# Performance work log

Hardware: AMD Instinct MI355X
Metric: run time of the kernel (lower is better)

## Reference

```python
import jax, jax.numpy as jnp
import numpy as np
from jax import lax

H = W = 224
FH = FW = 7          # backbone feature map spatial size
THRESH = 0.7
NUM_CLASSES = 14


def _conv(x, w, stride, pad):
    return lax.conv_general_dilated(
        x, w, (stride, stride), [(pad, pad), (pad, pad)],
        dimension_numbers=('NCHW', 'OIHW', 'NCHW'))


def backbone(x, w0, w1, w2, w3, fw, fb):
    # stand-in resnet50 trunk: 224 -> 56 -> 28 -> 14 -> 7, channels 3->64->512->1024->2048
    h = jax.nn.relu(_conv(x, w0, 4, 3))      # [B,64,56,56]
    h = jax.nn.relu(_conv(h, w1, 2, 1))      # [B,512,28,28]
    h = jax.nn.relu(_conv(h, w2, 2, 1))      # [B,1024,14,14]
    feat = jax.nn.relu(_conv(h, w3, 2, 1))   # [B,2048,7,7]
    pool = feat.max(axis=(2, 3))             # MaxPool2d(k=7,s=1) on 7x7 == global max -> [B,2048]
    out = jax.nn.sigmoid(pool @ fw.T + fb)   # fc + Sigmoid -> [B,14]
    return out, feat, pool


def attention_gen_patchs(img, fm):
    B, C, Hh, Ww = img.shape
    # per-sample channel-max abs heatmap, min-max normalized
    hm = jnp.max(jnp.abs(fm), axis=1)                              # [B,7,7]
    mn = hm.min(axis=(1, 2), keepdims=True)
    mx = hm.max(axis=(1, 2), keepdims=True)
    hm = (hm - mn) / (mx - mn)
    hm = jax.image.resize(hm, (B, Hh, Ww), method='bilinear')      # Resize((h,w))
    mask = (hm > THRESH).astype(jnp.int32)                         # [B,H,W]

    # largest 8-connected component: iterative max-label propagation
    ids = jnp.arange(1, Hh * Ww + 1, dtype=jnp.int32).reshape(1, Hh, Ww) * mask
    def body(_, lab):
        p = lax.reduce_window(lab, jnp.int32(0), lax.max, (1, 3, 3), (1, 1, 1), 'SAME')
        return p * mask
    labels = lax.fori_loop(0, Hh + Ww, body, ids)                  # [B,H,W] int32

    def counts_one(lab):
        c = jnp.zeros((Hh * Ww + 1,), jnp.int32).at[lab.reshape(-1)].add(1)
        return c.at[0].set(-1)                                     # ignore background
    counts = jax.vmap(counts_one)(labels)                          # [B,H*W+1]
    max_label = jnp.argmax(counts, axis=1)                         # [B]
    lcc = labels == max_label[:, None, None]                       # [B,H,W] bool

    # bbox of largest component (xmin/xmax over rows, ymin/ymax over cols)
    ri = jnp.arange(Hh); ci = jnp.arange(Ww)
    rows = lcc.any(axis=2); cols = lcc.any(axis=1)
    xmin = jnp.min(jnp.where(rows, ri[None, :], Hh), axis=1)
    xmax = jnp.max(jnp.where(rows, ri[None, :], -1), axis=1)       # inclusive; torch slice excludes it
    ymin = jnp.min(jnp.where(cols, ci[None, :], Ww), axis=1)
    ymax = jnp.max(jnp.where(cols, ci[None, :], -1), axis=1)
    ch = jnp.maximum(xmax - xmin, 1).astype(jnp.float32)           # crop height (exclusive slice)
    cw = jnp.maximum(ymax - ymin, 1).astype(jnp.float32)

    # bilinear resize of crop [xmin:xmax, ymin:ymax] back to (H,W), align_corners=False
    fy0 = xmin.astype(jnp.float32); fx0 = ymin.astype(jnp.float32)
    oy = (jnp.arange(Hh, dtype=jnp.float32) + 0.5)[None, :] * (ch[:, None] / Hh) + fy0[:, None] - 0.5
    ox = (jnp.arange(Ww, dtype=jnp.float32) + 0.5)[None, :] * (cw[:, None] / Ww) + fx0[:, None] - 0.5
    oy = jnp.clip(oy, fy0[:, None], jnp.maximum(fy0 + ch - 1.0, fy0)[:, None])
    ox = jnp.clip(ox, fx0[:, None], jnp.maximum(fx0 + cw - 1.0, fx0)[:, None])

    def sample_one(im, yy, xx):  # im [C,H,W]
        gy = jnp.broadcast_to(yy[:, None], (Hh, Ww))
        gx = jnp.broadcast_to(xx[None, :], (Hh, Ww))
        f = lambda chan: jax.scipy.ndimage.map_coordinates(chan, [gy, gx], order=1, mode='nearest')
        return jax.vmap(f)(im)
    return jax.vmap(sample_one)(img, oy, ox)                       # [B,C,H,W]


def bce(p, t):
    p = jnp.clip(p, 1e-7, 1.0 - 1e-7)
    return -jnp.mean(t * jnp.log(p) + (1.0 - t) * jnp.log1p(-p))


def setup_inputs() -> dict:
    key = jax.random.key(0)
    ks = jax.random.split(key, 20)
    B = 4
    def conv_w(k, o, i, s):
        return jax.random.normal(k, (o, i, s, s), jnp.float32) * np.sqrt(2.0 / (i * s * s)).astype(np.float32)
    def lin(k, o, i):
        return jax.random.normal(k, (o, i), jnp.float32) * np.sqrt(1.0 / i).astype(np.float32)
    inp = {
        'img': jax.random.uniform(ks[0], (B, 3, H, W), jnp.float32),
        'target': jax.random.uniform(ks[1], (B, NUM_CLASSES), jnp.float32),
        'gw0': conv_w(ks[2], 64, 3, 7), 'gw1': conv_w(ks[3], 512, 64, 3),
        'gw2': conv_w(ks[4], 1024, 512, 3), 'gw3': conv_w(ks[5], 2048, 1024, 3),
        'gfw': lin(ks[6], NUM_CLASSES, 2048), 'gfb': jnp.zeros((NUM_CLASSES,), jnp.float32),
        'lw0': conv_w(ks[7], 64, 3, 7), 'lw1': conv_w(ks[8], 512, 64, 3),
        'lw2': conv_w(ks[9], 1024, 512, 3), 'lw3': conv_w(ks[10], 2048, 1024, 3),
        'lfw': lin(ks[11], NUM_CLASSES, 2048), 'lfb': jnp.zeros((NUM_CLASSES,), jnp.float32),
        'fw': lin(ks[12], NUM_CLASSES, 2048 * 2), 'fb': jnp.zeros((NUM_CLASSES,), jnp.float32),
    }
    return inp


def reference(img, target, gw0, gw1, gw2, gw3, gfw, gfb,
              lw0, lw1, lw2, lw3, lfw, lfb, fw, fb):
    out_g, fm_g, pool_g = backbone(img, gw0, gw1, gw2, gw3, gfw, gfb)
    # patch generation is non-differentiable in the original (CPU/PIL round trip)
    patch = attention_gen_patchs(lax.stop_gradient(img), lax.stop_gradient(fm_g))
    out_l, _, pool_l = backbone(patch, lw0, lw1, lw2, lw3, lfw, lfb)
    out_f = jax.nn.sigmoid(jnp.concatenate([pool_g, pool_l], axis=1) @ fw.T + fb)
    gl = bce(out_g, target); ll = bce(out_l, target); fl = bce(out_f, target)
    loss = 0.8 * gl + 0.1 * ll + 0.1 * fl
    return loss, out_g, out_l, out_f, patch
```

## Files before the change

### kernel.cpp

```cpp
#include <hip/hip_runtime.h>
#include <math.h>

typedef __attribute__((ext_vector_type(8))) short short8m;
typedef __attribute__((ext_vector_type(4))) float f32x4;

__device__ inline unsigned short bf16_trunc(float f) {
  return (unsigned short)(__float_as_uint(f) >> 16);
}
__device__ inline unsigned short bf16_rte(float f) {
  unsigned u = __float_as_uint(f);
  u += 0x7fffu + ((u >> 16) & 1u);
  return (unsigned short)(u >> 16);
}
__device__ inline float bf16_tof(unsigned short h) {
  return __uint_as_float(((unsigned)h) << 16);
}
__device__ inline short8m* ldsPtr(unsigned short* base, int row, int byteInRow) {
  int off = (row * 128 + byteInRow) ^ ((row & 7) << 4);
  return (short8m*)((char*)base + off);
}
__device__ inline void gload16_lds(const void* g, void* d) {
  __builtin_amdgcn_global_load_lds((const __attribute__((address_space(1))) unsigned int*)g,
                                   (__attribute__((address_space(3))) unsigned int*)d, 16, 0, 0);
}

__global__ __launch_bounds__(256) void k_conv7(const float* __restrict__ x,
                                               const float* __restrict__ w,
                                               float* __restrict__ y) {
  __shared__ float ws[147];
  const int boc = blockIdx.y;
  const int oc = boc & 63;
  const int b = boc >> 6;
  for (int i = threadIdx.x; i < 147; i += 256) ws[i] = w[oc * 147 + i];
  __syncthreads();
  int px = blockIdx.x * 256 + threadIdx.x;
  if (px >= 56 * 56) return;
  int oy = px / 56, ox = px % 56;
  int iy0 = oy * 4 - 3, ix0 = ox * 4 - 3;
  float acc = 0.f;
  for (int c = 0; c < 3; ++c) {
    const float* xp = x + ((size_t)(b * 3 + c)) * 224 * 224;
    #pragma unroll
    for (int ky = 0; ky < 7; ++ky) {
      int iy = iy0 + ky;
      if ((unsigned)iy < 224u) {
        #pragma unroll
        for (int kx = 0; kx < 7; ++kx) {
          int ix = ix0 + kx;
          if ((unsigned)ix < 224u)
            acc += xp[iy * 224 + ix] * ws[c * 49 + ky * 7 + kx];
        }
      }
    }
  }
  y[((size_t)boc * 56 + oy) * 56 + ox] = fmaxf(acc, 0.f);
}

__global__ __launch_bounds__(256) void k_padw(const float* __restrict__ w,
                                              float* __restrict__ wp,
                                              int kreal, int ktot, int noc) {
  int i = blockIdx.x * 256 + threadIdx.x;
  if (i >= noc * ktot) return;
  int oc = i / ktot, k = i % ktot;
  wp[i] = (k < kreal) ? w[oc * kreal + k] : 0.f;
}

template <int CIN, int HIN, int WIN, int HOUT, int WOUT, int KH, int KW, int STR, int PAD, int KTOT>
__global__ __launch_bounds__(256) void k_im2col(const float* __restrict__ x,
                                                unsigned short* __restrict__ XgH,
                                                unsigned short* __restrict__ XgM) {
  constexpr int NPX = 4 * HOUT * WOUT;
  constexpr int K8 = KTOT / 8;
  constexpr int KK = KH * KW;
  int u = blockIdx.x * 256 + threadIdx.x;
  int pxin = u & 63;
  int k8 = (u >> 6) % K8;
  int pxblk = (u >> 6) / K8;
  int px = pxblk * 64 + pxin;
  if (px > NPX - 1) px = NPX - 1;
  const int hw = HOUT * WOUT;
  int pbv = px / hw;
  int r = px % hw;
  int py = r / WOUT, pxv = r % WOUT;
  short8m ph, pm;
  #pragma unroll
  for (int i = 0; i < 8; ++i) {
    int k = k8 * 8 + i;
    int ci = k / KK, tap = k - ci * KK;
    float v = 0.f;
    if (ci < CIN) {
      int iy = py * STR - PAD + tap / KW, ix = pxv * STR - PAD + (tap % KW);
      if ((unsigned)iy < (unsigned)HIN && (unsigned)ix < (unsigned)WIN)
        v = x[(((size_t)pbv * CIN + ci) * HIN + iy) * WIN + ix];
    }
    unsigned short hb = bf16_trunc(v);
    unsigned short mb = bf16_rte(v - bf16_tof(hb));
    ph[i] = (short)hb; pm[i] = (short)mb;
  }
  size_t off = (size_t)u * 8;
  *(short8m*)(XgH + off) = ph;
  *(short8m*)(XgM + off) = pm;
}

template <int COUT, int HOUT, int WOUT, int KTOT, int SPLIT, int OCT>
__global__ __launch_bounds__(OCT * 4) void k_gemmx(const unsigned short* __restrict__ XgH,
                                                   const unsigned short* __restrict__ XgM,
                                                   const float* __restrict__ wsrc,
                                                   float* __restrict__ part) {
  constexpr int NPX = 4 * HOUT * WOUT;
  constexpr int NPXB = (NPX + 63) / 64;
  constexpr int NOCB = COUT / OCT;
  constexpr int NWG = NPXB * NOCB * SPLIT;
  constexpr int KCH = KTOT / SPLIT;
  constexpr int NCH = KCH / 64;
  constexpr int NTHR = OCT * 4;
  constexpr int SLABS = 256 / OCT;
  __shared__ __align__(16) unsigned short XsH[4096];
  __shared__ __align__(16) unsigned short XsM[4096];
  __shared__ __align__(16) unsigned short WsH[OCT * 64];
  __shared__ __align__(16) unsigned short WsM[OCT * 64];
  __shared__ int pb[64], pyA[64], pxA[64];
  const int tid = threadIdx.x;
  const int flat = blockIdx.x;
  constexpr int q = NWG >> 3, r = NWG & 7;
  const int xc = flat & 7, of = flat >> 3;
  const int work = ((xc < r) ? xc * (q + 1) : r * (q + 1) + (xc - r) * q) + of;
  const int pxblk = work % NPXB;
  const int t2 = work / NPXB;
  const int oc0 = (t2 % NOCB) * OCT;
  const int spl = t2 / NOCB;
  if (tid < 64) {
    int p = pxblk * 64 + tid;
    if (p > NPX - 1) p = NPX - 1;
    int hw = HOUT * WOUT;
    pb[tid] = p / hw;
    int rr = p % hw;
    pyA[tid] = rr / WOUT;
    pxA[tid] = rr % WOUT;
  }
  f32x4 acc[4] = {};
  const int l = tid & 63, wv = tid >> 6;
  const int lr = l & 15, lh = l >> 4;
  __syncthreads();
  for (int ch = 0; ch < NCH; ++ch) {
    const int kbase = spl * KCH + ch * 64;
    const size_t tileOff = (size_t)pxblk * KTOT * 64 + (size_t)kbase * 64;
    #pragma unroll
    for (int t = 0; t < SLABS; ++t) {
      int ins = wv * SLABS + t;
      int pl = ins >> 3, ko = ins & 7;
      const unsigned short* g = (pl ? XgM : XgH) + tileOff + ko * 512 + l * 8;
      unsigned short* d = (pl ? XsM : XsH) + ko * 512;
      gload16_lds(g, d);
    }
    #pragma unroll
    for (int j = 0; j < 2; ++j) {
      int c = tid + NTHR * j;
      int oc = c >> 3, koct = c & 7;
      const float* wp = wsrc + (size_t)(oc0 + oc) * KTOT + kbase + koct * 8;
      float vv[8];
      *(float4*)&vv[0] = *(const float4*)wp;
      *(float4*)&vv[4] = *(const float4*)(wp + 4);
      short8m ph, pm;
      #pragma unroll
      for (int i = 0; i < 8; ++i) {
        unsigned short hb = bf16_trunc(vv[i]);
        unsigned short mb = bf16_rte(vv[i] - bf16_tof(hb));
        ph[i] = (short)hb; pm[i] = (short)mb;
      }
      *ldsPtr(WsH, oc, koct * 16) = ph;
      *ldsPtr(WsM, oc, koct * 16) = pm;
    }
    __syncthreads();
    #pragma unroll
    for (int ks = 0; ks < 2; ++ks) {
      const int kbyte = ks * 64 + lh * 16;
      short8m aH = *ldsPtr(WsH, wv * 16 + lr, kbyte);
      short8m aM = *ldsPtr(WsM, wv * 16 + lr, kbyte);
      const int xoff = (ks * 4 + lh) * 512;
      #pragma unroll
      for (int g4 = 0; g4 < 4; ++g4) {
        short8m bH = *(const short8m*)(XsH + xoff + (g4 * 16 + lr) * 8);
        short8m bM = *(const short8m*)(XsM + xoff + (g4 * 16 + lr) * 8);
        acc[g4] = __builtin_amdgcn_mfma_f32_16x16x32_bf16(aH, bH, acc[g4], 0, 0, 0);
        acc[g4] = __builtin_amdgcn_mfma_f32_16x16x32_bf16(aH, bM, acc[g4], 0, 0, 0);
        acc[g4] = __builtin_amdgcn_mfma_f32_16x16x32_bf16(aM, bH, acc[g4], 0, 0, 0);
      }
    }
    __syncthreads();
  }
  const size_t N = (size_t)4 * COUT * HOUT * WOUT;
  #pragma unroll
  for (int g4 = 0; g4 < 4; ++g4) {
    int pxl = g4 * 16 + lr;
    int pidx = pxblk * 64 + pxl;
    if (pidx < NPX) {
      #pragma unroll
      for (int rr = 0; rr < 4; ++rr) {
        int ocl = wv * 16 + lh * 4 + rr;
        float v = acc[g4][rr];
        if (SPLIT == 1) v = fmaxf(v, 0.f);
        part[(size_t)spl * N +
             (((size_t)pb[pxl] * COUT + (oc0 + ocl)) * HOUT + pyA[pxl]) * WOUT + pxA[pxl]] = v;
      }
    }
  }
}

template <int CIN, int HIN, int WIN, int COUT, int HOUT, int WOUT, int SPLIT>
__global__ __launch_bounds__(256) void k_convm(const float* __restrict__ x,
                                               const float* __restrict__ wsrc,
                                               float* __restrict__ part) {
  constexpr int NPX = 4 * HOUT * WOUT;
  constexpr int KTOT = (CIN * 9) / SPLIT;
  constexpr int NCH = KTOT / 64;
  __shared__ __align__(16) unsigned short Xs[2][64][64];
  __shared__ __align__(16) unsigned short Wsh[3][64][64];
  __shared__ int pb[64], pyA[64], pxA[64];
  const int tid = threadIdx.x;
  const int oc0 = blockIdx.y * 64, px0 = blockIdx.x * 64;
  const int spl = blockIdx.z;
  const int kg0 = spl * KTOT;
  if (tid < 64) {
    int p = px0 + tid;
    if (p > NPX - 1) p = NPX - 1;
    int hw = HOUT * WOUT;
    pb[tid] = p / hw;
    int r = p % hw;
    pyA[tid] = r / WOUT;
    pxA[tid] = r % WOUT;
  }
  f32x4 acc[4] = {};
  const int l = tid & 63, wv = tid >> 6;
  const int lr = l & 15, lh = l >> 4;
  __syncthreads();
  for (int ch = 0; ch < NCH; ++ch) {
    const int kbase = kg0 + ch * 64;
    #pragma unroll
    for (int j = 0; j < 2; ++j) {
      int c = tid + 256 * j;
      int oc = c >> 3, koct = c & 7;
      const float* wp = wsrc + (size_t)(oc0 + oc) * (CIN * 9) + kbase + koct * 8;
      float vv[8];
      *(float4*)&vv[0] = *(const float4*)wp;
      *(float4*)&vv[4] = *(const float4*)(wp + 4);
      short8m ph, pm, pl2;
      #pragma unroll
      for (int i = 0; i < 8; ++i) {
        unsigned short hb = bf16_trunc(vv[i]);
        float r = vv[i] - bf16_tof(hb);
        unsigned short mb = bf16_rte(r);
        float r2 = r - bf16_tof(mb);
        unsigned short lb = bf16_rte(r2);
        ph[i] = (short)hb; pm[i] = (short)mb; pl2[i] = (short)lb;
      }
      *ldsPtr(&Wsh[0][0][0], oc, koct * 16) = ph;
      *ldsPtr(&Wsh[1][0][0], oc, koct * 16) = pm;
      *ldsPtr(&Wsh[2][0][0], oc, koct * 16) = pl2;
    }
    #pragma unroll
    for (int j = 0; j < 2; ++j) {
      int c = tid + 256 * j;
      int px = c & 63, koct = c >> 6;
      int pbv = pb[px], py = pyA[px], pxv = pxA[px];
      float vv[8];
      #pragma unroll
      for (int i = 0; i < 8; ++i) {
        int k = kbase + koct * 8 + i;
        int ci = k / 9, tap = k - ci * 9;
        int iy = py * 2 - 1 + tap / 3, ix = pxv * 2 - 1 + (tap % 3);
        float v = 0.f;
        if ((unsigned)iy < (unsigned)HIN && (unsigned)ix < (unsigned)WIN)
          v = x[(((size_t)pbv * CIN + ci) * HIN + iy) * WIN + ix];
        vv[i] = v;
      }
      short8m ph, pm;
      #pragma unroll
      for (int i = 0; i < 8; ++i) {
        unsigned short hb = bf16_trunc(vv[i]);
        unsigned short mb = bf16_rte(vv[i] - bf16_tof(hb));
        ph[i] = (short)hb; pm[i] = (short)mb;
      }
      *ldsPtr(&Xs[0][0][0], px, koct * 16) = ph;
      *ldsPtr(&Xs[1][0][0], px, koct * 16) = pm;
    }
    __syncthreads();
    #pragma unroll
    for (int ks = 0; ks < 2; ++ks) {
      const int kbyte = ks * 64 + lh * 16;
      short8m aH = *ldsPtr(&Wsh[0][0][0], wv * 16 + lr, kbyte);
      short8m aM = *ldsPtr(&Wsh[1][0][0], wv * 16 + lr, kbyte);
      short8m aL = *ldsPtr(&Wsh[2][0][0], wv * 16 + lr, kbyte);
      #pragma unroll
      for (int g = 0; g < 4; ++g) {
        short8m bH = *ldsPtr(&Xs[0][0][0], g * 16 + lr, kbyte);
        short8m bM = *ldsPtr(&Xs[1][0][0], g * 16 + lr, kbyte);
        acc[g] = __builtin_amdgcn_mfma_f32_16x16x32_bf16(aH, bH, acc[g], 0, 0, 0);
        acc[g] = __builtin_amdgcn_mfma_f32_16x16x32_bf16(aH, bM, acc[g], 0, 0, 0);
        acc[g] = __builtin_amdgcn_mfma_f32_16x16x32_bf16(aM, bH, acc[g], 0, 0, 0);
        acc[g] = __builtin_amdgcn_mfma_f32_16x16x32_bf16(aM, bM, acc[g], 0, 0, 0);
        acc[g] = __builtin_amdgcn_mfma_f32_16x16x32_bf16(aL, bH, acc[g], 0, 0, 0);
      }
    }
    __syncthreads();
  }
  const size_t N = (size_t)4 * COUT * HOUT * WOUT;
  #pragma unroll
  for (int g = 0; g < 4; ++g) {
    int pxl = g * 16 + lr;
    int pidx = px0 + pxl;
    if (pidx < NPX) {
      #pragma unroll
      for (int r = 0; r < 4; ++r) {
        int ocl = wv * 16 + lh * 4 + r;
        part[(size_t)spl * N +
             (((size_t)pb[pxl] * COUT + (oc0 + ocl)) * HOUT + pyA[pxl]) * WOUT + pxA[pxl]] =
            acc[g][r];
      }
    }
  }
}

template <int SPLIT>
__global__ __launch_bounds__(256) void k_red(const float* __restrict__ part,
                                             float* __restrict__ y, int n) {
  for (int i = blockIdx.x * 256 + threadIdx.x; i < n; i += gridDim.x * 256) {
    float s = 0.f;
    #pragma unroll
    for (int sp = 0; sp < SPLIT; ++sp) s += part[(size_t)sp * n + i];
    y[i] = fmaxf(s, 0.f);
  }
}

__global__ __launch_bounds__(256) void k_pool(const float* __restrict__ feat,
                                              float* __restrict__ pool) {
  int idx = blockIdx.x * 256 + threadIdx.x;
  if (idx >= 8192) return;
  const float* fp = feat + (size_t)idx * 49;
  float m = fp[0];
  #pragma unroll
  for (int i = 1; i < 49; ++i) m = fmaxf(m, fp[i]);
  pool[idx] = m;
}

__global__ __launch_bounds__(256) void k_fcsig(const float* __restrict__ pool,
                                               const float* __restrict__ fw,
                                               const float* __restrict__ fb,
                                               float* __restrict__ outp) {
  __shared__ float red[256];
  const int blk = blockIdx.x;
  const int b = blk / 14, c = blk % 14;
  const int tid = threadIdx.x;
  float s = 0.f;
  for (int k = tid; k < 2048; k += 256) s += pool[b * 2048 + k] * fw[c * 2048 + k];
  red[tid] = s;
  __syncthreads();
  for (int st = 128; st > 0; st >>= 1) {
    if (tid < st) red[tid] += red[tid + st];
    __syncthreads();
  }
  if (tid == 0) outp[b * 14 + c] = 1.f / (1.f + expf(-(red[0] + fb[c])));
}

__global__ __launch_bounds__(256) void k_fcsig2(const float* __restrict__ poolg,
                                                const float* __restrict__ pooll,
                                                const float* __restrict__ fw,
                                                const float* __restrict__ fb,
                                                float* __restrict__ outp) {
  __shared__ float red[256];
  const int blk = blockIdx.x;
  const int b = blk / 14, c = blk % 14;
  const int tid = threadIdx.x;
  const float* w = fw + (size_t)c * 4096;
  float s = 0.f;
  for (int k = tid; k < 2048; k += 256) s += poolg[b * 2048 + k] * w[k];
  for (int k = tid; k < 2048; k += 256) s += pooll[b * 2048 + k] * w[2048 + k];
  red[tid] = s;
  __syncthreads();
  for (int st = 128; st > 0; st >>= 1) {
    if (tid < st) red[tid] += red[tid + st];
    __syncthreads();
  }
  if (tid == 0) outp[blk] = 1.f / (1.f + expf(-(red[0] + fb[c])));
}

__global__ __launch_bounds__(64) void k_loss(const float* __restrict__ target,
                                             float* __restrict__ dout) {
  __shared__ float red[64];
  const int tid = threadIdx.x;
  float term = 0.f;
  if (tid < 56) {
    float t = target[tid];
    float pg = dout[1 + tid], plo = dout[57 + tid], pf = dout[113 + tid];
    auto bce1 = [&](float pp) {
      pp = fminf(fmaxf(pp, 1e-7f), 1.f - 1e-7f);
      return -(t * logf(pp) + (1.f - t) * log1pf(-pp));
    };
    term = (0.8f * bce1(pg) + 0.1f * bce1(plo) + 0.1f * bce1(pf)) * (1.f / 56.f);
  }
  red[tid] = term;
  __syncthreads();
  for (int st = 32; st > 0; st >>= 1) {
    if (tid < st) red[tid] += red[tid + st];
    __syncthreads();
  }
  if (tid == 0) dout[0] = red[0];
}

__global__ __launch_bounds__(256) void k_hm7a(const float* __restrict__ feat,
                                              float* __restrict__ hmr) {
  __shared__ float red[256];
  const int b = blockIdx.x / 49, cell = blockIdx.x % 49;
  const int tid = threadIdx.x;
  float m = 0.f;
  for (int ch = tid; ch < 2048; ch += 256)
    m = fmaxf(m, fabsf(feat[((size_t)b * 2048 + ch) * 49 + cell]));
  red[tid] = m;
  __syncthreads();
  for (int st = 128; st > 0; st >>= 1) {
    if (tid < st) red[tid] = fmaxf(red[tid], red[tid + st]);
    __syncthreads();
  }
  if (tid == 0) hmr[b * 49 + cell] = red[0];
}

__global__ __launch_bounds__(64) void k_hm7b(const float* __restrict__ hmr,
                                             float* __restrict__ hm7) {
  __shared__ float h[49];
  const int b = blockIdx.x, tid = threadIdx.x;
  if (tid < 49) h[tid] = hmr[b * 49 + tid];
  __syncthreads();
  if (tid == 0) {
    float mn = h[0], mx = h[0];
    for (int i = 1; i < 49; ++i) {
      mn = fminf(mn, h[i]);
      mx = fmaxf(mx, h[i]);
    }
    for (int i = 0; i < 49; ++i) hm7[b * 49 + i] = (h[i] - mn) / (mx - mn);
  }
}

#define MAXR 8
#define NRUNS (224 * MAXR)
__global__ __launch_bounds__(256) void k_ccl(const float* __restrict__ hm7, float* __restrict__ bbox) {
  const int b = blockIdx.x, tid = threadIdx.x;
  __shared__ float h7[49];
  __shared__ short rx0[NRUNS], rx1[NRUNS];
  __shared__ short nr[224];
  __shared__ int lab[NRUNS];
  __shared__ int cnt[NRUNS], mid[NRUNS];
  __shared__ int rmn[NRUNS], rmx[NRUNS], cmn[NRUNS], cmx[NRUNS];
  __shared__ int chg, chg2;
  __shared__ int bestC[256], bestM[256], bestI[256];

  if (tid < 49) h7[tid] = hm7[b * 49 + tid];
  for (int i = tid; i < NRUNS; i += 256) {
    cnt[i] = 0; mid[i] = -1;
    rmn[i] = 1 << 30; rmx[i] = -1; cmn[i] = 1 << 30; cmx[i] = -1;
    lab[i] = i;
  }
  __syncthreads();
  if (tid < 224) {
    int yy = tid;
    float py = ((float)yy + 0.5f) * (7.f / 224.f) - 0.5f;
    py = fminf(fmaxf(py, 0.f), 6.f);
    int y0 = (int)floorf(py);
    if (y0 > 5) y0 = 5;
    float fy = py - (float)y0;
    int n = 0, start = -1;
    const int segLo[6] = {0, 48, 80, 112, 144, 176};
    const int segHi[6] = {48, 80, 112, 144, 176, 224};
    #pragma unroll
    for (int s = 0; s < 6; ++s) {
      float A = h7[y0 * 7 + s], B = h7[y0 * 7 + s + 1];
      float C = h7[(y0 + 1) * 7 + s], D = h7[(y0 + 1) * 7 + s + 1];
      for (int xx = segLo[s]; xx < segHi[s]; ++xx) {
        float px = ((float)xx + 0.5f) * (7.f / 224.f) - 0.5f;
        px = fminf(fmaxf(px, 0.f), 6.f);
        float fx = px - (float)s;
        float v = (1.f - fy) * ((1.f - fx) * A + fx * B) +
                  fy * ((1.f - fx) * C + fx * D);
        bool m = v > 0.7f;
        if (m && start < 0) start = xx;
        if (!m && start >= 0) {
          if (n < MAXR) { rx0[yy * MAXR + n] = (short)start; rx1[yy * MAXR + n] = (short)(xx - 1); n++; }
          start = -1;
        }
      }
    }
    if (start >= 0 && n < MAXR) { rx0[yy * MAXR + n] = (short)start; rx1[yy * MAXR + n] = 223; n++; }
    nr[yy] = (short)n;
  }
  __syncthreads();
  int myA0[7], myA1[7];
  bool myV[7];
  #pragma unroll
  for (int j = 0; j < 7; ++j) {
    int i = tid + j * 256;
    int yy = i >> 3, k = i & 7;
    bool v = (k < (int)nr[yy]);
    myV[j] = v;
    myA0[j] = v ? (int)rx0[i] : 0;
    myA1[j] = v ? (int)rx1[i] : 0;
  }
  for (int outer = 0; outer < 48; ++outer) {
    if (tid == 0) chg = 0;
    __syncthreads();
    bool any = false;
    #pragma unroll
    for (int j = 0; j < 7; ++j) {
      if (!myV[j]) continue;
      int i = tid + j * 256;
      int yy = i >> 3;
      int a0 = myA0[j], a1 = myA1[j];
      int ri = lab[i];
      if (yy > 0) {
        int n1 = nr[yy - 1];
        for (int kk = 0; kk < n1; ++kk) {
          int q = ((yy - 1) << 3) + kk;
          if (a0 <= rx1[q] + 1 && a1 >= rx0[q] - 1) {
            int rq = lab[q];
            if (rq < ri) { atomicMin(&lab[ri], rq); any = true; }
            else if (ri < rq) { atomicMin(&lab[rq], ri); any = true; }
          }
        }
      }
      if (yy < 223) {
        int n1 = nr[yy + 1];
        for (int kk = 0; kk < n1; ++kk) {
          int q = ((yy + 1) << 3) + kk;
          if (a0 <= rx1[q] + 1 && a1 >= rx0[q] - 1) {
            int rq = lab[q];
            if (rq < ri) { atomicMin(&lab[ri], rq); any = true; }
            else if (ri < rq) { atomicMin(&lab[rq], ri); any = true; }
          }
        }
      }
    }
    if (any) chg = 1;
    __syncthreads();
    for (int sc = 0; sc < 12; ++sc) {
      if (tid == 0) chg2 = 0;
      __syncthreads();
      bool a2 = false;
      #pragma unroll
      for (int j = 0; j < 7; ++j) {
        int i = tid + j * 256;
        int ll = lab[i];
        int l2 = lab[ll];
        if (l2 < ll) { lab[i] = l2; a2 = true; }
      }
      if (a2) chg2 = 1;
      __syncthreads();
      if (!chg2) break;
    }
    if (!chg) break;
  }
  for (int i = tid; i < NRUNS; i += 256) {
    int yy = i >> 3, k = i & 7;
    if (k >= (int)nr[yy]) continue;
    int r = lab[i];
    int a0 = rx0[i], a1 = rx1[i];
    atomicAdd(&cnt[r], a1 - a0 + 1);
    atomicMax(&mid[r], yy * 224 + a1 + 1);
    atomicMin(&rmn[r], yy);
    atomicMax(&rmx[r], yy);
    atomicMin(&cmn[r], a0);
    atomicMax(&cmx[r], a1);
  }
  __syncthreads();
  int bc = -1, bm = 0x7fffffff, bi = -1;
  for (int i = tid; i < NRUNS; i += 256) {
    if (cnt[i] > 0 && lab[i] == i) {
      if (cnt[i] > bc || (cnt[i] == bc && mid[i] < bm)) { bc = cnt[i]; bm = mid[i]; bi = i; }
    }
  }
  bestC[tid] = bc; bestM[tid] = bm; bestI[tid] = bi;
  __syncthreads();
  for (int st = 128; st > 0; st >>= 1) {
    if (tid < st) {
      if (bestC[tid + st] > bestC[tid] ||
          (bestC[tid + st] == bestC[tid] && bestM[tid + st] < bestM[tid])) {
        bestC[tid] = bestC[tid + st]; bestM[tid] = bestM[tid + st]; bestI[tid] = bestI[tid + st];
      }
    }
    __syncthreads();
  }
  if (tid == 0) {
    int bw = bestI[0];
    float fy0, chf, fx0, cwf;
    if (bw < 0) { fy0 = 224.f; chf = 1.f; fx0 = 224.f; cwf = 1.f; }
    else {
      int dr = rmx[bw] - rmn[bw]; if (dr < 1) dr = 1;
      int dc = cmx[bw] - cmn[bw]; if (dc < 1) dc = 1;
      fy0 = (float)rmn[bw]; chf = (float)dr;
      fx0 = (float)cmn[bw]; cwf = (float)dc;
    }
    bbox[b * 4 + 0] = fy0; bbox[b * 4 + 1] = chf;
    bbox[b * 4 + 2] = fx0; bbox[b * 4 + 3] = cwf;
  }
}

__global__ __launch_bounds__(256) void k_sample(const float* __restrict__ img,
                                                const float* __restrict__ bbox,
                                                float* __restrict__ patch_out,
                                                float* __restrict__ patch_ws) {
  int idx = blockIdx.x * 256 + threadIdx.x;
  if (idx >= 4 * 3 * 224 * 224) return;
  int b = idx / (3 * 224 * 224);
  int r = idx % (3 * 224 * 224);
  int c = r / (224 * 224);
  int p = r % (224 * 224);
  int oy = p / 224, ox = p % 224;
  float fy0 = bbox[b * 4 + 0], chf = bbox[b * 4 + 1];
  float fx0 = bbox[b * 4 + 2], cwf = bbox[b * 4 + 3];
  float gy = ((float)oy + 0.5f) * (chf / 224.f) + fy0 - 0.5f;
  float gx = ((float)ox + 0.5f) * (cwf / 224.f) + fx0 - 0.5f;
  gy = fminf(fmaxf(gy, fy0), fmaxf(fy0 + chf - 1.f, fy0));
  gx = fminf(fmaxf(gx, fx0), fmaxf(fx0 + cwf - 1.f, fx0));
  int y0 = (int)floorf(gy);
  int x0 = (int)floorf(gx);
  float fy = gy - (float)y0, fx = gx - (float)x0;
  int y0c = min(max(y0, 0), 223), y1c = min(max(y0 + 1, 0), 223);
  int x0c = min(max(x0, 0), 223), x1c = min(max(x0 + 1, 0), 223);
  const float* ip = img + ((size_t)b * 3 + c) * 224 * 224;
  float v00 = ip[y0c * 224 + x0c], v01 = ip[y0c * 224 + x1c];
  float v10 = ip[y1c * 224 + x0c], v11 = ip[y1c * 224 + x1c];
  float v = (1.f - fy) * ((1.f - fx) * v00 + fx * v01) + fy * ((1.f - fx) * v10 + fx * v11);
  patch_out[idx] = v;
  patch_ws[idx] = v;
}

extern "C" void kernel_launch(void* const* d_in, const int* in_sizes, int n_in,
                              void* d_out, int out_size, void* d_ws, size_t ws_size,
                              hipStream_t stream) {
  const float* img = (const float*)d_in[0];
  const float* target = (const float*)d_in[1];
  const float* gw0 = (const float*)d_in[2];
  const float* gw1 = (const float*)d_in[3];
  const float* gw2 = (const float*)d_in[4];
  const float* gw3 = (const float*)d_in[5];
  const float* gfw = (const float*)d_in[6];
  const float* gfb = (const float*)d_in[7];
  const float* lw0 = (const float*)d_in[8];
  const float* lw1 = (const float*)d_in[9];
  const float* lw2 = (const float*)d_in[10];
  const float* lw3 = (const float*)d_in[11];
  const float* lfw = (const float*)d_in[12];
  const float* lfb = (const float*)d_in[13];
  const float* fw = (const float*)d_in[14];
  const float* fb = (const float*)d_in[15];
  float* out = (float*)d_out;
  float* ws = (float*)d_ws;

  float* c1 = ws;
  float* c2 = c1 + 802816;
  float* c3 = c2 + 1605632;
  float* c4 = c3 + 802816;
  float* poolg = c4 + 401408;
  float* pooll = poolg + 8192;
  float* hm7 = pooll + 8192;
  float* hmr = hm7 + 196;
  float* bbox = hmr + 196;
  float* patch = ws + 3629568;
  float* part = ws + 4231680;
  float* Wp = part + 2800000;
  unsigned short* XgH = (unsigned short*)(ws + 7442944);
  unsigned short* XgM = XgH + 3840000;

  const bool fast = ws_size >= (size_t)45131776;

  dim3 g7(13, 256);
  const int rg2 = 2048, rg3 = 2048, rg4 = 1568;

  for (int pass = 0; pass < 2; ++pass) {
    const float* w0 = pass ? lw0 : gw0;
    const float* w1 = pass ? lw1 : gw1;
    const float* w2 = pass ? lw2 : gw2;
    const float* w3 = pass ? lw3 : gw3;
    const float* fwp = pass ? lfw : gfw;
    const float* fbp = pass ? lfb : gfb;
    const float* inp = pass ? patch : img;
    float* pool = pass ? pooll : poolg;
    float* outp = pass ? (out + 57) : (out + 1);

    if (fast) {
      k_padw<<<48, 256, 0, stream>>>(w0, Wp, 147, 192, 64);
      k_im2col<3, 224, 224, 56, 56, 7, 7, 4, 3, 192><<<1176, 256, 0, stream>>>(inp, XgH, XgM);
      k_gemmx<64, 56, 56, 192, 1, 64><<<196, 256, 0, stream>>>(XgH, XgM, Wp, c1);
      k_im2col<64, 56, 56, 28, 28, 3, 3, 2, 1, 576><<<882, 256, 0, stream>>>(c1, XgH, XgM);
      k_gemmx<512, 28, 28, 576, 1, 128><<<196, 512, 0, stream>>>(XgH, XgM, w1, c2);
      k_im2col<512, 28, 28, 14, 14, 3, 3, 2, 1, 4608><<<1872, 256, 0, stream>>>(c2, XgH, XgM);
      k_gemmx<1024, 14, 14, 4608, 4, 128><<<416, 512, 0, stream>>>(XgH, XgM, w2, part);
      k_red<4><<<rg3, 256, 0, stream>>>(part, c3, 802816);
      k_im2col<1024, 14, 14, 7, 7, 3, 3, 2, 1, 9216><<<1152, 256, 0, stream>>>(c3, XgH, XgM);
      k_gemmx<2048, 7, 7, 9216, 8, 128><<<512, 512, 0, stream>>>(XgH, XgM, w3, part);
      k_red<8><<<rg4, 256, 0, stream>>>(part, c4, 401408);
    } else {
      k_conv7<<<g7, 256, 0, stream>>>(inp, w0, c1);
      k_convm<64, 56, 56, 512, 28, 28, 1><<<dim3(49, 8, 1), 256, 0, stream>>>(c1, w1, part);
      k_red<1><<<rg2, 256, 0, stream>>>(part, c2, 1605632);
      k_convm<512, 28, 28, 1024, 14, 14, 4><<<dim3(13, 16, 4), 256, 0, stream>>>(c2, w2, part);
      k_red<4><<<rg3, 256, 0, stream>>>(part, c3, 802816);
      k_convm<1024, 14, 14, 2048, 7, 7, 8><<<dim3(4, 32, 8), 256, 0, stream>>>(c3, w3, part);
      k_red<8><<<rg4, 256, 0, stream>>>(part, c4, 401408);
    }
    k_pool<<<32, 256, 0, stream>>>(c4, pool);
    k_fcsig<<<56, 256, 0, stream>>>(pool, fwp, fbp, outp);

    if (pass == 0) {
      k_hm7a<<<196, 256, 0, stream>>>(c4, hmr);
      k_hm7b<<<4, 64, 0, stream>>>(hmr, hm7);
      k_ccl<<<4, 256, 0, stream>>>(hm7, bbox);
      k_sample<<<2352, 256, 0, stream>>>(img, bbox, out + 169, patch);
    }
  }
  k_fcsig2<<<56, 256, 0, stream>>>(poolg, pooll, fw, fb, out + 113);
  k_loss<<<1, 64, 0, stream>>>(target, out);
}
```

Before: 346.5 us.

## Double-buffer activation tile loads in k_gemmx to overlap with MFMA

```diff
diff --git a/kernel.cpp b/kernel.cpp
--- a/kernel.cpp
+++ b/kernel.cpp
@@ -115,8 +115,8 @@
   constexpr int NCH = KCH / 64;
   constexpr int NTHR = OCT * 4;
   constexpr int SLABS = 256 / OCT;
-  __shared__ __align__(16) unsigned short XsH[4096];
-  __shared__ __align__(16) unsigned short XsM[4096];
+  __shared__ __align__(16) unsigned short XsH[2][4096];
+  __shared__ __align__(16) unsigned short XsM[2][4096];
   __shared__ __align__(16) unsigned short WsH[OCT * 64];
   __shared__ __align__(16) unsigned short WsM[OCT * 64];
   __shared__ int pb[64], pyA[64], pxA[64];
@@ -141,18 +141,19 @@
   f32x4 acc[4] = {};
   const int l = tid & 63, wv = tid >> 6;
   const int lr = l & 15, lh = l >> 4;
-  __syncthreads();
+  const size_t tileBase = (size_t)pxblk * KTOT * 64 + (size_t)(spl * KCH) * 64;
+  __syncthreads();
+  #pragma unroll
+  for (int t = 0; t < SLABS; ++t) {
+    int ins = wv * SLABS + t;
+    int pl = ins >> 3, ko = ins & 7;
+    const unsigned short* g = (pl ? XgM : XgH) + tileBase + ko * 512 + l * 8;
+    unsigned short* d = (pl ? XsM[0] : XsH[0]) + ko * 512;
+    gload16_lds(g, d);
+  }
+  int cur = 0;
   for (int ch = 0; ch < NCH; ++ch) {
     const int kbase = spl * KCH + ch * 64;
-    const size_t tileOff = (size_t)pxblk * KTOT * 64 + (size_t)kbase * 64;
-    #pragma unroll
-    for (int t = 0; t < SLABS; ++t) {
-      int ins = wv * SLABS + t;
-      int pl = ins >> 3, ko = ins & 7;
-      const unsigned short* g = (pl ? XgM : XgH) + tileOff + ko * 512 + l * 8;
-      unsigned short* d = (pl ? XsM : XsH) + ko * 512;
-      gload16_lds(g, d);
-    }
     #pragma unroll
     for (int j = 0; j < 2; ++j) {
       int c = tid + NTHR * j;
@@ -171,7 +172,20 @@
       *ldsPtr(WsH, oc, koct * 16) = ph;
       *ldsPtr(WsM, oc, koct * 16) = pm;
     }
-    __syncthreads();
+    if (ch + 1 < NCH) {
+      const size_t tOff = tileBase + (size_t)(ch + 1) * 64 * 64;
+      #pragma unroll
+      for (int t = 0; t < SLABS; ++t) {
+        int ins = wv * SLABS + t;
+        int pl = ins >> 3, ko = ins & 7;
+        const unsigned short* g = (pl ? XgM : XgH) + tOff + ko * 512 + l * 8;
+        unsigned short* d = (pl ? XsM[cur ^ 1] : XsH[cur ^ 1]) + ko * 512;
+        gload16_lds(g, d);
+      }
+    }
+    asm volatile("s_waitcnt lgkmcnt(0)" ::: "memory");
+    __builtin_amdgcn_s_barrier();
+    __builtin_amdgcn_sched_barrier(0);
     #pragma unroll
     for (int ks = 0; ks < 2; ++ks) {
       const int kbyte = ks * 64 + lh * 16;
@@ -180,14 +194,17 @@
       const int xoff = (ks * 4 + lh) * 512;
       #pragma unroll
       for (int g4 = 0; g4 < 4; ++g4) {
-        short8m bH = *(const short8m*)(XsH + xoff + (g4 * 16 + lr) * 8);
-        short8m bM = *(const short8m*)(XsM + xoff + (g4 * 16 + lr) * 8);
+        short8m bH = *(const short8m*)(XsH[cur] + xoff + (g4 * 16 + lr) * 8);
+        short8m bM = *(const short8m*)(XsM[cur] + xoff + (g4 * 16 + lr) * 8);
         acc[g4] = __builtin_amdgcn_mfma_f32_16x16x32_bf16(aH, bH, acc[g4], 0, 0, 0);
         acc[g4] = __builtin_amdgcn_mfma_f32_16x16x32_bf16(aH, bM, acc[g4], 0, 0, 0);
         acc[g4] = __builtin_amdgcn_mfma_f32_16x16x32_bf16(aM, bH, acc[g4], 0, 0, 0);
       }
     }
-    __syncthreads();
+    asm volatile("s_waitcnt lgkmcnt(0)" ::: "memory");
+    __builtin_amdgcn_s_barrier();
+    __builtin_amdgcn_sched_barrier(0);
+    cur ^= 1;
   }
   const size_t N = (size_t)4 * COUT * HOUT * WOUT;
   #pragma unroll
@@ -279,6 +296,7 @@
       for (int i = 0; i < 8; ++i) {
         unsigned short hb = bf16_trunc(vv[i]);
         unsigned short mb = bf16_rte(vv[i] - bf16_tof(hb));
+        ph[i] = (short)hb; pm[i] = (short)pm[i];
         ph[i] = (short)hb; pm[i] = (short)mb;
       }
       *ldsPtr(&Xs[0][0][0], px, koct * 16) = ph;
```

After: 348.8 us. Within noise of the previous version (+0.7%).
